# Kernel tuning notes

Hardware: AMD Instinct MI355X
Metric: run time of the kernel (lower is better)

The kernel has to match this reference:

```python
import jax, jax.numpy as jnp
import numpy as np

H = 2048      # hidden_size
I = 8192      # intermediate_size
NH = 16       # num_heads
HD = H // NH  # head_dim
EPS = 1e-6


def setup_inputs() -> dict:
    key = jax.random.key(0)
    ks = jax.random.split(key, 10)
    s = 0.02
    return {
        "hidden_states": jax.random.normal(ks[0], (2, 2048, H), dtype=jnp.float32),
        "wq": jax.random.normal(ks[1], (H, H), dtype=jnp.float32) * s,
        "wk": jax.random.normal(ks[2], (H, H), dtype=jnp.float32) * s,
        "wv": jax.random.normal(ks[3], (H, H), dtype=jnp.float32) * s,
        "wo": jax.random.normal(ks[4], (H, H), dtype=jnp.float32) * s,
        "w_gate": jax.random.normal(ks[5], (H, I), dtype=jnp.float32) * s,
        "w_up": jax.random.normal(ks[6], (H, I), dtype=jnp.float32) * s,
        "w_down": jax.random.normal(ks[7], (I, H), dtype=jnp.float32) * s,
        "ln1_w": jnp.ones((H,), dtype=jnp.float32),
        "ln2_w": jnp.ones((H,), dtype=jnp.float32),
    }


def rmsnorm(x, w):
    xf = x.astype(jnp.float32)
    var = jnp.mean(xf * xf, axis=-1, keepdims=True)
    return w * (xf * jax.lax.rsqrt(var + EPS)).astype(x.dtype)


def reference(hidden_states, wq, wk, wv, wo, w_gate, w_up, w_down, ln1_w, ln2_w):
    b, s, _ = hidden_states.shape
    residual = hidden_states
    x = rmsnorm(hidden_states, ln1_w)

    # attention (no RoPE, no causal mask, per source)
    q = (x @ wq).reshape(b, s, NH, HD)
    k = (x @ wk).reshape(b, s, NH, HD)
    v = (x @ wv).reshape(b, s, NH, HD)
    scores = jnp.einsum('bqhd,bkhd->bhqk', q, k) / jnp.sqrt(jnp.float32(HD))
    attn = jax.nn.softmax(scores, axis=-1)
    out = jnp.einsum('bhqk,bkhd->bqhd', attn, v).reshape(b, s, H)
    hidden = residual + out @ wo

    residual = hidden
    y = rmsnorm(hidden, ln2_w)
    gate = jax.nn.silu(y @ w_gate)
    up = y @ w_up
    return residual + (gate * up) @ w_down
```

## Files before the change

### kernel.cpp

```cpp
#include <hip/hip_runtime.h>
#include <hip/hip_bf16.h>

#define HDIM 2048
#define IDIM 8192
#define NHEADS 16
#define HEADD 128
#define BATCH 2
#define SEQ 2048
#define MTOK 4096

typedef unsigned short u16;
typedef __bf16 bf16x8 __attribute__((ext_vector_type(8)));
typedef float f32x4 __attribute__((ext_vector_type(4)));
typedef float f32x16 __attribute__((ext_vector_type(16)));
typedef unsigned short u16x8 __attribute__((ext_vector_type(8)));
typedef unsigned int u32x2 __attribute__((ext_vector_type(2)));
typedef unsigned int u32x4 __attribute__((ext_vector_type(4)));
typedef unsigned int uv2 __attribute__((ext_vector_type(2)));

__device__ __forceinline__ u16 f2b(float f) {
  unsigned u = __builtin_bit_cast(unsigned, f);
  u += 0x7FFFu + ((u >> 16) & 1u);
  return (u16)(u >> 16);
}
__device__ __forceinline__ float b2f(u16 b) {
  unsigned u = ((unsigned)b) << 16;
  return __builtin_bit_cast(float, u);
}
__device__ __forceinline__ void gl_lds16(const void* g, void* l) {
  auto gp = (const __attribute__((address_space(1))) unsigned int*)((unsigned long long)g);
  auto lp = (__attribute__((address_space(3))) unsigned int*)((unsigned)(unsigned long long)l);
  __builtin_amdgcn_global_load_lds(gp, lp, 16, 0, 0);
}
__device__ __forceinline__ unsigned cvtpk(float lo, float hi) {
  unsigned r;
  asm("v_cvt_pk_bf16_f32 %0, %1, %2" : "=v"(r) : "v"(lo), "v"(hi));
  return r;
}

__global__ __launch_bounds__(256) void wtrans_k(const float* __restrict__ W, u16* __restrict__ Wt,
                                                int K, int N, int rowoff) {
  __shared__ float t[64][65];
  int n0 = blockIdx.x * 64, k0 = blockIdx.y * 64;
  int tid = threadIdx.x;
  int kr = tid >> 4, nc = (tid & 15) * 4;
#pragma unroll
  for (int p = 0; p < 4; p++) {
    float4 v = *(const float4*)&W[(size_t)(k0 + p * 16 + kr) * N + n0 + nc];
    t[nc + 0][p * 16 + kr] = v.x;
    t[nc + 1][p * 16 + kr] = v.y;
    t[nc + 2][p * 16 + kr] = v.z;
    t[nc + 3][p * 16 + kr] = v.w;
  }
  __syncthreads();
  int n = tid >> 2, kq = (tid & 3) * 16;
  u16 tmp[16];
#pragma unroll
  for (int i = 0; i < 16; i++) tmp[i] = f2b(t[n][kq + i]);
  *(u16x8*)&Wt[(size_t)(rowoff + n0 + n) * K + k0 + kq] = *(u16x8*)&tmp[0];
  *(u16x8*)&Wt[(size_t)(rowoff + n0 + n) * K + k0 + kq + 8] = *(u16x8*)&tmp[8];
}

__global__ __launch_bounds__(256) void vtrans_k(const u16* __restrict__ qkv, u16* __restrict__ vt) {
  __shared__ u16 t[32][33];
  int s0 = blockIdx.x * 32, d0 = blockIdx.y * 32, bh = blockIdx.z;
  int b = bh >> 4, h = bh & 15;
  int tx = threadIdx.x, ty = threadIdx.y;
#pragma unroll
  for (int i = 0; i < 4; i++)
    t[ty + i * 8][tx] = qkv[(size_t)(b * SEQ + s0 + ty + i * 8) * 6144 + 4096 + h * HEADD + d0 + tx];
  __syncthreads();
#pragma unroll
  for (int i = 0; i < 4; i++)
    vt[(size_t)(bh * HEADD + d0 + ty + i * 8) * SEQ + s0 + tx] = t[tx][ty + i * 8];
}

__global__ __launch_bounds__(256) void rmsnorm_k(const float* __restrict__ X, const float* __restrict__ W,
                                                 u16* __restrict__ O) {
  int row = blockIdx.x;
  int tid = threadIdx.x;
  const float* x = X + (size_t)row * HDIM;
  float4 v0 = ((const float4*)x)[tid * 2];
  float4 v1 = ((const float4*)x)[tid * 2 + 1];
  float ss = v0.x * v0.x + v0.y * v0.y + v0.z * v0.z + v0.w * v0.w
           + v1.x * v1.x + v1.y * v1.y + v1.z * v1.z + v1.w * v1.w;
#pragma unroll
  for (int off = 32; off > 0; off >>= 1) ss += __shfl_down(ss, off);
  __shared__ float red[4];
  if ((tid & 63) == 0) red[tid >> 6] = ss;
  __syncthreads();
  float rs = rsqrtf((red[0] + red[1] + red[2] + red[3]) * (1.0f / HDIM) + 1e-6f);
  const float* w = W + tid * 8;
  u16* o = O + (size_t)row * HDIM + tid * 8;
  float vals[8] = {v0.x, v0.y, v0.z, v0.w, v1.x, v1.y, v1.z, v1.w};
#pragma unroll
  for (int j = 0; j < 8; j++) o[j] = f2b(w[j] * vals[j] * rs);
}

template <int EPI>
__global__ __launch_bounds__(512, 2) void gemm_w(const u16* __restrict__ A, const u16* __restrict__ Bt,
                                                 int M, int N, int K,
                                                 u16* __restrict__ Cb, float* __restrict__ Cf,
                                                 const float* __restrict__ Res, u16* __restrict__ Gm) {
  __shared__ char lds[131072];
  const int tid = threadIdx.x;
  const int lane = tid & 63, w = tid >> 6;
  const int wm = w >> 2, wn = w & 3;
  const int bid = blockIdx.y * gridDim.x + blockIdx.x;
  const int xcd = bid & 7, idx = bid >> 3;
  const int round = idx >> 4, j = idx & 15;
  const int nsy4 = gridDim.y >> 2;
  const int st = round * 8 + xcd;
  const int sx = st / nsy4, syi = st % nsy4;
  const int by = syi * 4 + (j & 3), bx = sx * 4 + (j >> 2);
  const int m0 = by * 256, n0 = bx * 256;
  const int NT = K >> 6;

  const int srow = w * 8 + (lane >> 3);
  const int kko = ((lane & 7) ^ (lane >> 3)) * 8;
  const u16* Asrc = A + (size_t)(m0 + srow) * K + kko;
  const u16* Bsrc = Bt + (size_t)(n0 + srow) * K + kko;
  const int wofs = w * 1024;

#define STAGE_AH(buf, kt, h)                                                          \
  {                                                                                   \
    gl_lds16(Asrc + ((size_t)((h) * 128) * K) + (size_t)(kt) * 64,                    \
             lds + (buf) * 65536 + (h) * 16384 + wofs);                               \
    gl_lds16(Asrc + ((size_t)((h) * 128 + 64) * K) + (size_t)(kt) * 64,               \
             lds + (buf) * 65536 + (h) * 16384 + 8192 + wofs);                        \
  }
#define STAGE_BH(buf, kt, h)                                                          \
  {                                                                                   \
    gl_lds16(Bsrc + ((size_t)((h) * 128) * K) + (size_t)(kt) * 64,                    \
             lds + (buf) * 65536 + 32768 + (h) * 16384 + wofs);                       \
    gl_lds16(Bsrc + ((size_t)((h) * 128 + 64) * K) + (size_t)(kt) * 64,               \
             lds + (buf) * 65536 + 32768 + (h) * 16384 + 8192 + wofs);                \
  }
#define LG0 { asm volatile("s_waitcnt lgkmcnt(0)" ::: "memory"); __builtin_amdgcn_sched_barrier(0); }

  const int l15 = lane & 15, l4 = lane >> 4;
  const int kq0 = ((l4) ^ (l15 & 7)) << 4;
  const int kq1 = ((4 + l4) ^ (l15 & 7)) << 4;
  const int abase = wm * 16384 + l15 * 128;
  const int bbase = 32768 + (wn >> 1) * 16384 + ((wn & 1) * 64 + l15) * 128;

  const f32x4 fz = {0.f, 0.f, 0.f, 0.f};
  f32x4 acc[8][4];
#pragma unroll
  for (int i = 0; i < 8; i++)
#pragma unroll
    for (int jj = 0; jj < 4; jj++) acc[i][jj] = fz;
  bf16x8 af[4], bfr[4];

  STAGE_AH(0, 0, 0);
  STAGE_AH(0, 0, 1);
  STAGE_BH(0, 0, 0);
  STAGE_BH(0, 0, 1);
  STAGE_AH(1, 1, 0);
  STAGE_BH(1, 1, 0);
  asm volatile("s_waitcnt vmcnt(4)" ::: "memory");
  __builtin_amdgcn_s_barrier();

  for (int t = 0; t < NT; ++t) {
    const int buf = t & 1, nbuf = buf ^ 1;
    const char* Lb = lds + buf * 65536;
    const int t1 = (t + 1 < NT) ? t + 1 : NT - 1;
    const int t2 = (t + 2 < NT) ? t + 2 : NT - 1;
#pragma unroll
    for (int mf = 0; mf < 4; mf++) af[mf] = *(const bf16x8*)(Lb + abase + mf * 2048 + kq0);
#pragma unroll
    for (int nf = 0; nf < 4; nf++) bfr[nf] = *(const bf16x8*)(Lb + bbase + nf * 2048 + kq0);
    STAGE_AH(nbuf, t1, 1);
    STAGE_BH(nbuf, t1, 1);
    __builtin_amdgcn_s_barrier();
    LG0;
    __builtin_amdgcn_s_setprio(1);
#pragma unroll
    for (int mf = 0; mf < 4; mf++)
#pragma unroll
      for (int nf = 0; nf < 4; nf++)
        acc[mf][nf] = __builtin_amdgcn_mfma_f32_16x16x32_bf16(af[mf], bfr[nf], acc[mf][nf], 0, 0, 0);
    __builtin_amdgcn_s_setprio(0);
    __builtin_amdgcn_s_barrier();
#pragma unroll
    for (int mf = 0; mf < 4; mf++) af[mf] = *(const bf16x8*)(Lb + abase + (mf + 4) * 2048 + kq0);
    __builtin_amdgcn_s_barrier();
    LG0;
    __builtin_amdgcn_s_setprio(1);
#pragma unroll
    for (int mf = 0; mf < 4; mf++)
#pragma unroll
      for (int nf = 0; nf < 4; nf++)
        acc[mf + 4][nf] = __builtin_amdgcn_mfma_f32_16x16x32_bf16(af[mf], bfr[nf], acc[mf + 4][nf], 0, 0, 0);
    __builtin_amdgcn_s_setprio(0);
    __builtin_amdgcn_s_barrier();
#pragma unroll
    for (int mf = 0; mf < 4; mf++) af[mf] = *(const bf16x8*)(Lb + abase + mf * 2048 + kq1);
#pragma unroll
    for (int nf = 0; nf < 4; nf++) bfr[nf] = *(const bf16x8*)(Lb + bbase + nf * 2048 + kq1);
    __builtin_amdgcn_s_barrier();
    LG0;
    __builtin_amdgcn_s_setprio(1);
#pragma unroll
    for (int mf = 0; mf < 4; mf++)
#pragma unroll
      for (int nf = 0; nf < 4; nf++)
        acc[mf][nf] = __builtin_amdgcn_mfma_f32_16x16x32_bf16(af[mf], bfr[nf], acc[mf][nf], 0, 0, 0);
    __builtin_amdgcn_s_setprio(0);
    __builtin_amdgcn_s_barrier();
#pragma unroll
    for (int mf = 0; mf < 4; mf++) af[mf] = *(const bf16x8*)(Lb + abase + (mf + 4) * 2048 + kq1);
    STAGE_AH(buf, t2, 0);
    STAGE_BH(buf, t2, 0);
    __builtin_amdgcn_s_barrier();
    LG0;
    __builtin_amdgcn_s_setprio(1);
#pragma unroll
    for (int mf = 0; mf < 4; mf++)
#pragma unroll
      for (int nf = 0; nf < 4; nf++)
        acc[mf + 4][nf] = __builtin_amdgcn_mfma_f32_16x16x32_bf16(af[mf], bfr[nf], acc[mf + 4][nf], 0, 0, 0);
    __builtin_amdgcn_s_setprio(0);
    asm volatile("s_waitcnt vmcnt(4)" ::: "memory");
    __builtin_amdgcn_s_barrier();
  }
  asm volatile("s_waitcnt vmcnt(0)" ::: "memory");

  const int r0 = l4 * 4;
#pragma unroll
  for (int mf = 0; mf < 8; mf++) {
#pragma unroll
    for (int jr = 0; jr < 4; jr++) {
      const int m = m0 + wm * 128 + mf * 16 + r0 + jr;
#pragma unroll
      for (int nf = 0; nf < 4; nf++) {
        const int n = n0 + wn * 64 + nf * 16 + l15;
        float v = acc[mf][nf][jr];
        size_t idx = (size_t)m * N + n;
        if (EPI == 0) {
          Cb[idx] = f2b(v);
        } else if (EPI == 1) {
          float sg = v / (1.f + __expf(-v));
          Cb[idx] = f2b(sg);
        } else if (EPI == 2) {
          float gv = b2f(Gm[idx]);
          Gm[idx] = f2b(gv * v);
        } else {
          Cf[idx] = Res[idx] + v;
        }
      }
    }
  }
#undef STAGE_AH
#undef STAGE_BH
#undef LG0
}

template <int EPI>
__global__ __launch_bounds__(512, 2) void gemm256(const u16* __restrict__ A, const u16* __restrict__ Bt,
                                                  int M, int N, int K,
                                                  u16* __restrict__ Cb, float* __restrict__ Cf,
                                                  const float* __restrict__ Res, u16* __restrict__ Gm) {
  __shared__ char lds[98304];
  const int tid = threadIdx.x;
  const int lane = tid & 63, w = tid >> 6;
  const int wm = w >> 1, wn = w & 1;
  const int nwg = gridDim.x * gridDim.y;
  const int bid = blockIdx.y * gridDim.x + blockIdx.x;
  const int swz = (bid & 7) * (nwg >> 3) + (bid >> 3);
  const int bx = swz % gridDim.x, by = swz / gridDim.x;
  const int n0 = bx * 128, m0 = by * 256;
  const int NT = K >> 6;

  const int r8 = lane >> 3, s8 = lane & 7;
  const int slog8 = (s8 ^ r8) * 8;
  const u16* Abase = A + (size_t)(m0 + w * 8 + r8) * K + slog8;
  const u16* Bbase = Bt + (size_t)(n0 + w * 8 + r8) * K + slog8;
  const int stA = w * 1024;

#define STAGE_A(buf, kt, h)                                                        \
  {                                                                                \
    const u16* s_ = Abase + (size_t)(h) * 128 * K + (size_t)(kt) * 64;             \
    gl_lds16(s_, lds + (buf) * 49152 + (h) * 16384 + stA);                         \
    gl_lds16(s_ + 64 * (size_t)K, lds + (buf) * 49152 + (h) * 16384 + stA + 8192); \
  }
#define STAGE_B(buf, kt)                                                     \
  {                                                                          \
    const u16* s_ = Bbase + (size_t)(kt) * 64;                               \
    gl_lds16(s_, lds + (buf) * 49152 + 32768 + stA);                         \
    gl_lds16(s_ + 64 * (size_t)K, lds + (buf) * 49152 + 32768 + stA + 8192); \
  }
#define LG0 { asm volatile("s_waitcnt lgkmcnt(0)" ::: "memory"); __builtin_amdgcn_sched_barrier(0); }

  const int l15 = lane & 15, l4 = lane >> 4;
  const int kq0 = (l4 * 16) ^ ((lane & 7) << 4);
  const int kq1 = (64 + l4 * 16) ^ ((lane & 7) << 4);
  const int aro = (wm >> 1) * 16384 + ((wm & 1) * 64 + l15) * 128;
  const int bro = 32768 + (wn * 64 + l15) * 128;

  const f32x4 fz = {0.f, 0.f, 0.f, 0.f};
  f32x4 acc[4][4];
#pragma unroll
  for (int i = 0; i < 4; i++)
#pragma unroll
    for (int j = 0; j < 4; j++) acc[i][j] = fz;
  bf16x8 af[4][2], bfr[4][2];

  STAGE_A(0, 0, 0);
  STAGE_A(0, 0, 1);
  STAGE_B(0, 0);
  STAGE_A(1, 1, 0);
  STAGE_A(1, 1, 1);
  asm volatile("s_waitcnt vmcnt(4)" ::: "memory");
  __builtin_amdgcn_s_barrier();

  for (int t = 0; t < NT; ++t) {
    const int buf = t & 1;
    const char* Lb = lds + buf * 49152;
    const int t1 = (t + 1 < NT) ? t + 1 : NT - 1;
    const int t2 = (t + 2 < NT) ? t + 2 : NT - 1;
    if (wm < 2) {
#pragma unroll
      for (int mf = 0; mf < 4; mf++) {
        af[mf][0] = *(const bf16x8*)(Lb + aro + mf * 2048 + kq0);
        af[mf][1] = *(const bf16x8*)(Lb + aro + mf * 2048 + kq1);
      }
    } else {
#pragma unroll
      for (int mf = 0; mf < 4; mf++)
        af[mf][0] = *(const bf16x8*)(Lb + aro + mf * 2048 + kq0);
    }
#pragma unroll
    for (int nf = 0; nf < 4; nf++)
      bfr[nf][0] = *(const bf16x8*)(Lb + bro + nf * 2048 + kq0);
    STAGE_B((t + 1) & 1, t1);
    __builtin_amdgcn_s_barrier();
    LG0;
    __builtin_amdgcn_s_setprio(1);
#pragma unroll
    for (int nf = 0; nf < 4; nf++) {
      acc[0][nf] = __builtin_amdgcn_mfma_f32_16x16x32_bf16(af[0][0], bfr[nf][0], acc[0][nf], 0, 0, 0);
      acc[1][nf] = __builtin_amdgcn_mfma_f32_16x16x32_bf16(af[1][0], bfr[nf][0], acc[1][nf], 0, 0, 0);
    }
    __builtin_amdgcn_s_setprio(0);
    __builtin_amdgcn_s_barrier();
    if (wm >= 2) {
#pragma unroll
      for (int mf = 0; mf < 4; mf++)
        af[mf][1] = *(const bf16x8*)(Lb + aro + mf * 2048 + kq1);
    }
#pragma unroll
    for (int nf = 0; nf < 4; nf++)
      bfr[nf][1] = *(const bf16x8*)(Lb + bro + nf * 2048 + kq1);
    STAGE_A(buf, t2, 0);
    __builtin_amdgcn_s_barrier();
    LG0;
    __builtin_amdgcn_s_setprio(1);
#pragma unroll
    for (int nf = 0; nf < 4; nf++) {
      acc[2][nf] = __builtin_amdgcn_mfma_f32_16x16x32_bf16(af[2][0], bfr[nf][0], acc[2][nf], 0, 0, 0);
      acc[3][nf] = __builtin_amdgcn_mfma_f32_16x16x32_bf16(af[3][0], bfr[nf][0], acc[3][nf], 0, 0, 0);
    }
    __builtin_amdgcn_s_setprio(0);
    __builtin_amdgcn_s_barrier();
    STAGE_A(buf, t2, 1);
    __builtin_amdgcn_s_barrier();
    LG0;
    __builtin_amdgcn_s_setprio(1);
#pragma unroll
    for (int nf = 0; nf < 4; nf++) {
      acc[0][nf] = __builtin_amdgcn_mfma_f32_16x16x32_bf16(af[0][1], bfr[nf][1], acc[0][nf], 0, 0, 0);
      acc[1][nf] = __builtin_amdgcn_mfma_f32_16x16x32_bf16(af[1][1], bfr[nf][1], acc[1][nf], 0, 0, 0);
    }
    __builtin_amdgcn_s_setprio(0);
    __builtin_amdgcn_s_barrier();
    __builtin_amdgcn_s_setprio(1);
#pragma unroll
    for (int nf = 0; nf < 4; nf++) {
      acc[2][nf] = __builtin_amdgcn_mfma_f32_16x16x32_bf16(af[2][1], bfr[nf][1], acc[2][nf], 0, 0, 0);
      acc[3][nf] = __builtin_amdgcn_mfma_f32_16x16x32_bf16(af[3][1], bfr[nf][1], acc[3][nf], 0, 0, 0);
    }
    __builtin_amdgcn_s_setprio(0);
    asm volatile("s_waitcnt vmcnt(4)" ::: "memory");
    __builtin_amdgcn_s_barrier();
  }
  asm volatile("s_waitcnt vmcnt(0)" ::: "memory");

  const int r0 = l4 * 4;
#pragma unroll
  for (int mf = 0; mf < 4; mf++) {
#pragma unroll
    for (int j = 0; j < 4; j++) {
      const int m = m0 + wm * 64 + mf * 16 + r0 + j;
#pragma unroll
      for (int nf = 0; nf < 4; nf++) {
        const int n = n0 + wn * 64 + nf * 16 + l15;
        float v = acc[mf][nf][j];
        size_t idx = (size_t)m * N + n;
        if (EPI == 0) {
          Cb[idx] = f2b(v);
        } else if (EPI == 1) {
          float sg = v / (1.f + __expf(-v));
          Cb[idx] = f2b(sg);
        } else if (EPI == 2) {
          float gv = b2f(Gm[idx]);
          Gm[idx] = f2b(gv * v);
        } else {
          Cf[idx] = Res[idx] + v;
        }
      }
    }
  }
#undef STAGE_A
#undef STAGE_B
#undef LG0
}

__global__ __launch_bounds__(512, 2) void attn_k(const u16* __restrict__ qkv, const u16* __restrict__ vt,
                                                 u16* __restrict__ out) {
  __shared__ char Kl[2][16384];
  __shared__ char Vl[2][16384];
  int tid = threadIdx.x, lane = tid & 63, w = tid >> 6;
  int bid = blockIdx.y * 8 + blockIdx.x;
  int swz = (bid & 7) * 32 + (bid >> 3);
  int qb = swz & 7, bh = swz >> 3;
  int b = bh >> 4, h = bh & 15;
  int l31 = lane & 31, hi = lane >> 5;
  const float c = 0.088388347648318447f * 1.4426950408889634f;
  const float RT = 90.51f;

  const int qrow = qb * 256 + w * 32 + l31;
  bf16x8 q[8];
  {
    const u16* qp = qkv + (size_t)(b * SEQ + qrow) * 6144 + h * HEADD + hi * 8;
#pragma unroll
    for (int dt = 0; dt < 8; dt++) q[dt] = *(const bf16x8*)(qp + dt * 16);
  }
  f32x16 o[4];
#pragma unroll
  for (int i = 0; i < 4; i++)
#pragma unroll
    for (int j = 0; j < 16; j++) o[i][j] = 0.f;
  float mrow = -1e30f, lrow = 0.f;

#define ASTAGE(buf, t)                                                                     \
  {                                                                                        \
    int kv0_ = (t) * 64;                                                                   \
    _Pragma("unroll") for (int i = 0; i < 2; i++) {                                        \
      int r = w * 8 + i * 4 + (lane >> 4);                                                 \
      int col = ((lane & 15) ^ (r & 15)) * 8;                                              \
      const u16* src = qkv + (size_t)(b * SEQ + kv0_ + r) * 6144 + HDIM + h * HEADD + col; \
      gl_lds16(src, &Kl[buf][(w * 8 + i * 4) * 256]);                                      \
    }                                                                                      \
    _Pragma("unroll") for (int i = 0; i < 2; i++) {                                        \
      int d = w * 16 + i * 8 + (lane >> 3);                                                \
      int col = ((lane & 7) ^ (d & 7)) * 8;                                                \
      const u16* src = vt + (size_t)(bh * HEADD + d) * SEQ + kv0_ + col;                   \
      gl_lds16(src, &Vl[buf][(w * 16 + i * 8) * 128]);                                     \
    }                                                                                      \
  }

  ASTAGE(0, 0);
  __syncthreads();

  for (int t = 0; t < SEQ / 64; t++) {
    const int buf = t & 1;
    if (t + 1 < SEQ / 64) ASTAGE(buf ^ 1, t + 1);
    const char* Kb = &Kl[buf][0];
    const char* Vb = &Vl[buf][0];
    f32x16 s0, s1;
#pragma unroll
    for (int j = 0; j < 16; j++) { s0[j] = 0.f; s1[j] = 0.f; }
    const int ksl = l31 & 15;
    __builtin_amdgcn_s_setprio(1);
#pragma unroll
    for (int dt = 0; dt < 8; dt++) {
      bf16x8 k0 = *(const bf16x8*)(Kb + (l31)*256 + (((dt * 2 + hi) ^ ksl) << 4));
      bf16x8 k1 = *(const bf16x8*)(Kb + (32 + l31) * 256 + (((dt * 2 + hi) ^ ksl) << 4));
      s0 = __builtin_amdgcn_mfma_f32_32x32x16_bf16(k0, q[dt], s0, 0, 0, 0);
      s1 = __builtin_amdgcn_mfma_f32_32x32x16_bf16(k1, q[dt], s1, 0, 0, 0);
    }
    __builtin_amdgcn_s_setprio(0);
    float m8[8];
#pragma unroll
    for (int g = 0; g < 4; g++) {
      m8[g] = fmaxf(fmaxf(s0[4 * g], s0[4 * g + 1]), fmaxf(s0[4 * g + 2], s0[4 * g + 3]));
      m8[4 + g] = fmaxf(fmaxf(s1[4 * g], s1[4 * g + 1]), fmaxf(s1[4 * g + 2], s1[4 * g + 3]));
    }
    float vmax = fmaxf(fmaxf(fmaxf(m8[0], m8[1]), fmaxf(m8[2], m8[3])),
                       fmaxf(fmaxf(m8[4], m8[5]), fmaxf(m8[6], m8[7])));
    {
      uv2 pr = __builtin_amdgcn_permlane32_swap(__builtin_bit_cast(unsigned, vmax),
                                                __builtin_bit_cast(unsigned, vmax), false, false);
      vmax = fmaxf(__builtin_bit_cast(float, pr[0]), __builtin_bit_cast(float, pr[1]));
    }
    if (__any(vmax > mrow + RT)) {
      float mnew = fmaxf(mrow, vmax);
      float alpha = exp2f((mrow - mnew) * c);
      mrow = mnew;
      lrow *= alpha;
#pragma unroll
      for (int i = 0; i < 4; i++)
#pragma unroll
        for (int j = 0; j < 16; j++) o[i][j] *= alpha;
    }
    const float mc = mrow * c;
    float r4[4] = {0.f, 0.f, 0.f, 0.f};
#pragma unroll
    for (int j = 0; j < 16; j++) {
      s0[j] = exp2f(s0[j] * c - mc);
      r4[j & 3] += s0[j];
    }
#pragma unroll
    for (int j = 0; j < 16; j++) {
      s1[j] = exp2f(s1[j] * c - mc);
      r4[j & 3] += s1[j];
    }
    float rsum = (r4[0] + r4[1]) + (r4[2] + r4[3]);
    {
      uv2 pr = __builtin_amdgcn_permlane32_swap(__builtin_bit_cast(unsigned, rsum),
                                                __builtin_bit_cast(unsigned, rsum), false, false);
      rsum = __builtin_bit_cast(float, pr[0]) + __builtin_bit_cast(float, pr[1]);
    }
    lrow += rsum;
    bf16x8 pa[4];
#pragma unroll
    for (int half = 0; half < 2; half++) {
      const f32x16& sv = half ? s1 : s0;
#pragma unroll
      for (int blk = 0; blk < 2; blk++) {
        int base = blk * 8;
        unsigned A = cvtpk(sv[base + 0], sv[base + 1]);
        unsigned B = cvtpk(sv[base + 2], sv[base + 3]);
        unsigned C = cvtpk(sv[base + 4], sv[base + 5]);
        unsigned D = cvtpk(sv[base + 6], sv[base + 7]);
        uv2 ac = __builtin_amdgcn_permlane32_swap(A, C, false, false);
        uv2 bd = __builtin_amdgcn_permlane32_swap(B, D, false, false);
        u32x4 w4;
        w4[0] = ac[0]; w4[1] = bd[0]; w4[2] = ac[1]; w4[3] = bd[1];
        pa[half * 2 + blk] = __builtin_bit_cast(bf16x8, w4);
      }
    }
    __builtin_amdgcn_s_setprio(1);
#pragma unroll
    for (int dt4 = 0; dt4 < 4; dt4++) {
      const char* vbase = Vb + (dt4 * 32 + l31) * 128;
      const int vsl = l31 & 7;
#pragma unroll
      for (int ks = 0; ks < 4; ks++) {
        bf16x8 vb = *(const bf16x8*)(vbase + (((ks * 2 + hi) ^ vsl) << 4));
        o[dt4] = __builtin_amdgcn_mfma_f32_32x32x16_bf16(vb, pa[ks], o[dt4], 0, 0, 0);
      }
    }
    __builtin_amdgcn_s_setprio(0);
    __syncthreads();
  }
#undef ASTAGE

  const float linv = 1.0f / lrow;
  u16* orow = out + (size_t)(b * SEQ + qrow) * HDIM + h * HEADD;
#pragma unroll
  for (int dt4 = 0; dt4 < 4; dt4++) {
#pragma unroll
    for (int g = 0; g < 4; g++) {
      u32x2 st;
      st[0] = cvtpk(o[dt4][4 * g + 0] * linv, o[dt4][4 * g + 1] * linv);
      st[1] = cvtpk(o[dt4][4 * g + 2] * linv, o[dt4][4 * g + 3] * linv);
      *(u32x2*)(orow + dt4 * 32 + 8 * g + 4 * hi) = st;
    }
  }
}

extern "C" void kernel_launch(void* const* d_in, const int* in_sizes, int n_in,
                              void* d_out, int out_size, void* d_ws, size_t ws_size,
                              hipStream_t stream) {
  const float* hs  = (const float*)d_in[0];
  const float* wq  = (const float*)d_in[1];
  const float* wk  = (const float*)d_in[2];
  const float* wv  = (const float*)d_in[3];
  const float* wo  = (const float*)d_in[4];
  const float* wg  = (const float*)d_in[5];
  const float* wu  = (const float*)d_in[6];
  const float* wd  = (const float*)d_in[7];
  const float* ln1 = (const float*)d_in[8];
  const float* ln2 = (const float*)d_in[9];
  char* ws = (char*)d_ws;
  u16*   wqkvT = (u16*)(ws);
  u16*   woT   = (u16*)(ws + 25165824ull);
  u16*   wgT   = (u16*)(ws + 33554432ull);
  u16*   wuT   = (u16*)(ws + 67108864ull);
  u16*   wdT   = (u16*)(ws + 100663296ull);
  u16*   xb    = (u16*)(ws + 134217728ull);
  float* hid   = (float*)(ws + 150994944ull);
  u16*   qkv   = (u16*)(ws + 184549376ull);
  u16*   vtb   = (u16*)(ws + 234881024ull);
  u16*   attn  = (u16*)(ws + 251658368ull);
  u16*   g     = qkv;

  wtrans_k<<<dim3(32, 32), 256, 0, stream>>>(wq, wqkvT, HDIM, HDIM, 0);
  wtrans_k<<<dim3(32, 32), 256, 0, stream>>>(wk, wqkvT, HDIM, HDIM, 2048);
  wtrans_k<<<dim3(32, 32), 256, 0, stream>>>(wv, wqkvT, HDIM, HDIM, 4096);
  wtrans_k<<<dim3(32, 32), 256, 0, stream>>>(wo, woT, HDIM, HDIM, 0);
  wtrans_k<<<dim3(128, 32), 256, 0, stream>>>(wg, wgT, HDIM, IDIM, 0);
  wtrans_k<<<dim3(128, 32), 256, 0, stream>>>(wu, wuT, HDIM, IDIM, 0);
  wtrans_k<<<dim3(32, 128), 256, 0, stream>>>(wd, wdT, IDIM, HDIM, 0);

  rmsnorm_k<<<MTOK, 256, 0, stream>>>(hs, ln1, xb);
  gemm_w<0><<<dim3(24, 16), 512, 0, stream>>>(xb, wqkvT, MTOK, 6144, HDIM, qkv, nullptr, nullptr, nullptr);
  vtrans_k<<<dim3(64, 4, 32), dim3(32, 8), 0, stream>>>(qkv, vtb);
  attn_k<<<dim3(8, 32), 512, 0, stream>>>(qkv, vtb, attn);
  gemm256<3><<<dim3(16, 16), 512, 0, stream>>>(attn, woT, MTOK, HDIM, HDIM, nullptr, hid, hs, nullptr);
  rmsnorm_k<<<MTOK, 256, 0, stream>>>(hid, ln2, xb);
  gemm_w<1><<<dim3(32, 16), 512, 0, stream>>>(xb, wgT, MTOK, IDIM, HDIM, g, nullptr, nullptr, nullptr);
  gemm_w<2><<<dim3(32, 16), 512, 0, stream>>>(xb, wuT, MTOK, IDIM, HDIM, nullptr, nullptr, nullptr, g);
  gemm256<3><<<dim3(16, 16), 512, 0, stream>>>(g, wdT, MTOK, HDIM, IDIM, nullptr, (float*)d_out, hid, nullptr);
}
```

Measured before the change: 773.4 us.

## Fuse gate and up GEMMs with SwiGLU epilogue; merge weight transposes into one launch

Replaces the separate gate GEMM (silu epilogue) and up GEMM (read-multiply-write epilogue) with one kernel. It loads a shared A tile once and computes both gate and up accumulators for a 256x128 output tile, then writes silu(g)*u directly. This removes a second pass over the activations and the bf16 round trip of the intermediate gate tensor. The seven weight-transpose launches are also merged into a single launch. The trade-off is higher register pressure from the two accumulator sets and a new hand-pipelined schedule with narrower N tiles.

```diff
diff --git a/kernel.cpp b/kernel.cpp
--- a/kernel.cpp
+++ b/kernel.cpp
@@ -38,10 +38,41 @@
   return r;
 }
 
-__global__ __launch_bounds__(256) void wtrans_k(const float* __restrict__ W, u16* __restrict__ Wt,
-                                                int K, int N, int rowoff) {
+__global__ __launch_bounds__(256) void wtrans_all(const float* __restrict__ wq, const float* __restrict__ wk,
+                                                  const float* __restrict__ wv, const float* __restrict__ wo,
+                                                  const float* __restrict__ wg, const float* __restrict__ wu,
+                                                  const float* __restrict__ wd,
+                                                  u16* __restrict__ wqkvT, u16* __restrict__ woT,
+                                                  u16* __restrict__ wgT, u16* __restrict__ wuT,
+                                                  u16* __restrict__ wdT) {
+  int bidf = blockIdx.x;
+  const float* W;
+  u16* Wt;
+  int K, N, rowoff, bx, by;
+  if (bidf < 3072) {
+    int s = bidf >> 10, r = bidf & 1023;
+    W = s == 0 ? wq : (s == 1 ? wk : wv);
+    Wt = wqkvT; K = 2048; N = 2048; rowoff = s * 2048;
+    bx = r & 31; by = r >> 5;
+  } else if (bidf < 4096) {
+    int r = bidf - 3072;
+    W = wo; Wt = woT; K = 2048; N = 2048; rowoff = 0;
+    bx = r & 31; by = r >> 5;
+  } else if (bidf < 8192) {
+    int r = bidf - 4096;
+    W = wg; Wt = wgT; K = 2048; N = 8192; rowoff = 0;
+    bx = r & 127; by = r >> 7;
+  } else if (bidf < 12288) {
+    int r = bidf - 8192;
+    W = wu; Wt = wuT; K = 2048; N = 8192; rowoff = 0;
+    bx = r & 127; by = r >> 7;
+  } else {
+    int r = bidf - 12288;
+    W = wd; Wt = wdT; K = 8192; N = 2048; rowoff = 0;
+    bx = r & 31; by = r >> 5;
+  }
   __shared__ float t[64][65];
-  int n0 = blockIdx.x * 64, k0 = blockIdx.y * 64;
+  int n0 = bx * 64, k0 = by * 64;
   int tid = threadIdx.x;
   int kr = tid >> 4, nc = (tid & 15) * 4;
 #pragma unroll
@@ -95,6 +126,155 @@
   float vals[8] = {v0.x, v0.y, v0.z, v0.w, v1.x, v1.y, v1.z, v1.w};
 #pragma unroll
   for (int j = 0; j < 8; j++) o[j] = f2b(w[j] * vals[j] * rs);
+}
+
+__global__ __launch_bounds__(512, 2) void gemm_fgu(const u16* __restrict__ A, const u16* __restrict__ Bg,
+                                                   const u16* __restrict__ Bu, u16* __restrict__ G) {
+  __shared__ char lds[131072];
+  const int tid = threadIdx.x, lane = tid & 63, w = tid >> 6;
+  const int wm = w >> 2, wn = w & 3;
+  const int bid = blockIdx.y * 64 + blockIdx.x;
+  const int swz = (bid & 7) * 128 + (bid >> 3);
+  const int bx = swz & 63, by = swz >> 6;
+  const int m0 = by * 256, n0 = bx * 128;
+  const int NT = 32;
+
+  const int srow = w * 8 + (lane >> 3);
+  const int kko = ((lane & 7) ^ (lane >> 3)) * 8;
+  const u16* Asrc = A + (size_t)(m0 + srow) * 2048 + kko;
+  const u16* Bgsrc = Bg + (size_t)(n0 + srow) * 2048 + kko;
+  const u16* Busrc = Bu + (size_t)(n0 + srow) * 2048 + kko;
+  const int wofs = w * 1024;
+
+#define SA0(buf, kt)                                                        \
+  {                                                                         \
+    gl_lds16(Asrc + (kt) * 64, lds + (buf) * 65536 + wofs);                 \
+    gl_lds16(Asrc + 64 * 2048 + (kt) * 64, lds + (buf) * 65536 + 8192 + wofs); \
+  }
+#define SA1(buf, kt)                                                              \
+  {                                                                               \
+    gl_lds16(Asrc + 128 * 2048 + (kt) * 64, lds + (buf) * 65536 + 16384 + wofs);  \
+    gl_lds16(Asrc + 192 * 2048 + (kt) * 64, lds + (buf) * 65536 + 24576 + wofs);  \
+  }
+#define SBG(buf, kt)                                                              \
+  {                                                                               \
+    gl_lds16(Bgsrc + (kt) * 64, lds + (buf) * 65536 + 32768 + wofs);              \
+    gl_lds16(Bgsrc + 64 * 2048 + (kt) * 64, lds + (buf) * 65536 + 40960 + wofs);  \
+  }
+#define SBU(buf, kt)                                                              \
+  {                                                                               \
+    gl_lds16(Busrc + (kt) * 64, lds + (buf) * 65536 + 49152 + wofs);              \
+    gl_lds16(Busrc + 64 * 2048 + (kt) * 64, lds + (buf) * 65536 + 57344 + wofs);  \
+  }
+#define LG0 { asm volatile("s_waitcnt lgkmcnt(0)" ::: "memory"); __builtin_amdgcn_sched_barrier(0); }
+
+  const int l15 = lane & 15, l4 = lane >> 4;
+  const int kq0 = ((l4) ^ (l15 & 7)) << 4;
+  const int kq1 = ((4 + l4) ^ (l15 & 7)) << 4;
+  const int abase = (wm * 128 + l15) * 128;
+  const int gbase = 32768 + (wn * 32 + l15) * 128;
+  const int ubase = 49152 + (wn * 32 + l15) * 128;
+
+  const f32x4 fz = {0.f, 0.f, 0.f, 0.f};
+  f32x4 ag[8][2], au[8][2];
+#pragma unroll
+  for (int i = 0; i < 8; i++)
+#pragma unroll
+    for (int j = 0; j < 2; j++) { ag[i][j] = fz; au[i][j] = fz; }
+  bf16x8 af[8], bgf[2], buf2[2];
+
+  SA0(0, 0);
+  SBG(0, 0);
+  SA1(0, 0);
+  SBU(0, 0);
+  asm volatile("s_waitcnt vmcnt(2)" ::: "memory");
+  __builtin_amdgcn_s_barrier();
+
+  for (int t = 0; t < NT; ++t) {
+    const int buf = t & 1, nb = buf ^ 1;
+    const char* Lb = lds + buf * 65536;
+    const int t1 = (t + 1 < NT) ? t + 1 : NT - 1;
+#pragma unroll
+    for (int mf = 0; mf < 8; mf++) af[mf] = *(const bf16x8*)(Lb + abase + mf * 2048 + kq0);
+    bgf[0] = *(const bf16x8*)(Lb + gbase + kq0);
+    bgf[1] = *(const bf16x8*)(Lb + gbase + 2048 + kq0);
+    SA0(nb, t1);
+    SBG(nb, t1);
+    __builtin_amdgcn_s_barrier();
+    LG0;
+    __builtin_amdgcn_s_setprio(1);
+#pragma unroll
+    for (int mf = 0; mf < 8; mf++) {
+      ag[mf][0] = __builtin_amdgcn_mfma_f32_16x16x32_bf16(af[mf], bgf[0], ag[mf][0], 0, 0, 0);
+      ag[mf][1] = __builtin_amdgcn_mfma_f32_16x16x32_bf16(af[mf], bgf[1], ag[mf][1], 0, 0, 0);
+    }
+    __builtin_amdgcn_s_setprio(0);
+    asm volatile("s_waitcnt vmcnt(4)" ::: "memory");
+    __builtin_amdgcn_s_barrier();
+    buf2[0] = *(const bf16x8*)(Lb + ubase + kq0);
+    buf2[1] = *(const bf16x8*)(Lb + ubase + 2048 + kq0);
+    SA1(nb, t1);
+    __builtin_amdgcn_s_barrier();
+    LG0;
+    __builtin_amdgcn_s_setprio(1);
+#pragma unroll
+    for (int mf = 0; mf < 8; mf++) {
+      au[mf][0] = __builtin_amdgcn_mfma_f32_16x16x32_bf16(af[mf], buf2[0], au[mf][0], 0, 0, 0);
+      au[mf][1] = __builtin_amdgcn_mfma_f32_16x16x32_bf16(af[mf], buf2[1], au[mf][1], 0, 0, 0);
+    }
+    __builtin_amdgcn_s_setprio(0);
+    __builtin_amdgcn_s_barrier();
+#pragma unroll
+    for (int mf = 0; mf < 8; mf++) af[mf] = *(const bf16x8*)(Lb + abase + mf * 2048 + kq1);
+    bgf[0] = *(const bf16x8*)(Lb + gbase + kq1);
+    bgf[1] = *(const bf16x8*)(Lb + gbase + 2048 + kq1);
+    __builtin_amdgcn_s_barrier();
+    LG0;
+    __builtin_amdgcn_s_setprio(1);
+#pragma unroll
+    for (int mf = 0; mf < 8; mf++) {
+      ag[mf][0] = __builtin_amdgcn_mfma_f32_16x16x32_bf16(af[mf], bgf[0], ag[mf][0], 0, 0, 0);
+      ag[mf][1] = __builtin_amdgcn_mfma_f32_16x16x32_bf16(af[mf], bgf[1], ag[mf][1], 0, 0, 0);
+    }
+    __builtin_amdgcn_s_setprio(0);
+    __builtin_amdgcn_s_barrier();
+    buf2[0] = *(const bf16x8*)(Lb + ubase + kq1);
+    buf2[1] = *(const bf16x8*)(Lb + ubase + 2048 + kq1);
+    SBU(nb, t1);
+    __builtin_amdgcn_s_barrier();
+    LG0;
+    __builtin_amdgcn_s_setprio(1);
+#pragma unroll
+    for (int mf = 0; mf < 8; mf++) {
+      au[mf][0] = __builtin_amdgcn_mfma_f32_16x16x32_bf16(af[mf], buf2[0], au[mf][0], 0, 0, 0);
+      au[mf][1] = __builtin_amdgcn_mfma_f32_16x16x32_bf16(af[mf], buf2[1], au[mf][1], 0, 0, 0);
+    }
+    __builtin_amdgcn_s_setprio(0);
+    asm volatile("s_waitcnt vmcnt(2)" ::: "memory");
+    __builtin_amdgcn_s_barrier();
+  }
+  asm volatile("s_waitcnt vmcnt(0)" ::: "memory");
+
+#pragma unroll
+  for (int mf = 0; mf < 8; mf++) {
+#pragma unroll
+    for (int jr = 0; jr < 4; jr++) {
+      const int m = m0 + wm * 128 + mf * 16 + l4 * 4 + jr;
+#pragma unroll
+      for (int nf = 0; nf < 2; nf++) {
+        const int n = n0 + wn * 32 + nf * 16 + l15;
+        float g = ag[mf][nf][jr];
+        float u = au[mf][nf][jr];
+        float sg = g / (1.f + __expf(-g));
+        G[(size_t)m * IDIM + n] = f2b(sg * u);
+      }
+    }
+  }
+#undef SA0
+#undef SA1
+#undef SBG
+#undef SBU
+#undef LG0
 }
 
 template <int EPI>
@@ -239,13 +419,7 @@
         size_t idx = (size_t)m * N + n;
         if (EPI == 0) {
           Cb[idx] = f2b(v);
-        } else if (EPI == 1) {
-          float sg = v / (1.f + __expf(-v));
-          Cb[idx] = f2b(sg);
-        } else if (EPI == 2) {
-          float gv = b2f(Gm[idx]);
-          Gm[idx] = f2b(gv * v);
-        } else {
+        } else if (EPI == 3) {
           Cf[idx] = Res[idx] + v;
         }
       }
@@ -399,13 +573,7 @@
         size_t idx = (size_t)m * N + n;
         if (EPI == 0) {
           Cb[idx] = f2b(v);
-        } else if (EPI == 1) {
-          float sg = v / (1.f + __expf(-v));
-          Cb[idx] = f2b(sg);
-        } else if (EPI == 2) {
-          float gv = b2f(Gm[idx]);
-          Gm[idx] = f2b(gv * v);
-        } else {
+        } else if (EPI == 3) {
           Cf[idx] = Res[idx] + v;
         }
       }
@@ -597,13 +765,7 @@
   u16*   attn  = (u16*)(ws + 251658368ull);
   u16*   g     = qkv;
 
-  wtrans_k<<<dim3(32, 32), 256, 0, stream>>>(wq, wqkvT, HDIM, HDIM, 0);
-  wtrans_k<<<dim3(32, 32), 256, 0, stream>>>(wk, wqkvT, HDIM, HDIM, 2048);
-  wtrans_k<<<dim3(32, 32), 256, 0, stream>>>(wv, wqkvT, HDIM, HDIM, 4096);
-  wtrans_k<<<dim3(32, 32), 256, 0, stream>>>(wo, woT, HDIM, HDIM, 0);
-  wtrans_k<<<dim3(128, 32), 256, 0, stream>>>(wg, wgT, HDIM, IDIM, 0);
-  wtrans_k<<<dim3(128, 32), 256, 0, stream>>>(wu, wuT, HDIM, IDIM, 0);
-  wtrans_k<<<dim3(32, 128), 256, 0, stream>>>(wd, wdT, IDIM, HDIM, 0);
+  wtrans_all<<<16384, 256, 0, stream>>>(wq, wk, wv, wo, wg, wu, wd, wqkvT, woT, wgT, wuT, wdT);
 
   rmsnorm_k<<<MTOK, 256, 0, stream>>>(hs, ln1, xb);
   gemm_w<0><<<dim3(24, 16), 512, 0, stream>>>(xb, wqkvT, MTOK, 6144, HDIM, qkv, nullptr, nullptr, nullptr);
@@ -611,7 +773,6 @@
   attn_k<<<dim3(8, 32), 512, 0, stream>>>(qkv, vtb, attn);
   gemm256<3><<<dim3(16, 16), 512, 0, stream>>>(attn, woT, MTOK, HDIM, HDIM, nullptr, hid, hs, nullptr);
   rmsnorm_k<<<MTOK, 256, 0, stream>>>(hid, ln2, xb);
-  gemm_w<1><<<dim3(32, 16), 512, 0, stream>>>(xb, wgT, MTOK, IDIM, HDIM, g, nullptr, nullptr, nullptr);
-  gemm_w<2><<<dim3(32, 16), 512, 0, stream>>>(xb, wuT, MTOK, IDIM, HDIM, nullptr, nullptr, nullptr, g);
+  gemm_fgu<<<dim3(64, 16), 512, 0, stream>>>(xb, wgT, wuT, g);
   gemm256<3><<<dim3(16, 16), 512, 0, stream>>>(g, wdT, MTOK, HDIM, IDIM, nullptr, (float*)d_out, hid, nullptr);
 }
```

Result: faster. 726.7 us (-6.0%).
